# Performance work log

Measured on AMD Instinct MI355X. Metric: run time of the kernel, lower is better.

## Reference

```python
import jax, jax.numpy as jnp
import numpy as np

B, S, V, L, H, NH, NL = 4, 256, 64, 10, 128, 8, 3
DH = H // NH
LP1 = L + 1


def setup_inputs() -> dict:
    key = jax.random.key(0)
    ks = jax.random.split(key, 18)
    sc = 1.0 / np.sqrt(H)
    return {
        "x": jax.random.normal(ks[0], (B, S, V), jnp.float32),
        "adjacency_logits": jax.random.normal(ks[1], (V, V, LP1), jnp.float32) * 0.1,
        "var_emb": jax.random.normal(ks[2], (V, H), jnp.float32),
        "temp_emb": jax.random.normal(ks[3], (LP1, H), jnp.float32),
        "mech_W": jax.random.normal(ks[4], (V, NL, H, H), jnp.float32) * sc,
        "mech_b": jax.random.normal(ks[5], (V, NL, H), jnp.float32) * 0.01,
        "ln_g": jnp.ones((V, NL, H), jnp.float32),
        "ln_b": jnp.zeros((V, NL, H), jnp.float32),
        "Wq": jax.random.normal(ks[6], (V, H, H), jnp.float32) * sc,
        "Wk": jax.random.normal(ks[7], (V, H, H), jnp.float32) * sc,
        "Wv": jax.random.normal(ks[8], (V, H, H), jnp.float32) * sc,
        "Wo": jax.random.normal(ks[9], (V, H, H), jnp.float32) * sc,
        "bq": jnp.zeros((V, H), jnp.float32),
        "bk": jnp.zeros((V, H), jnp.float32),
        "bv": jnp.zeros((V, H), jnp.float32),
        "bo": jnp.zeros((V, H), jnp.float32),
        "out_W": jax.random.normal(ks[10], (V, H), jnp.float32) * sc,
        "out_b": jnp.zeros((V,), jnp.float32),
    }


def reference(x, adjacency_logits, var_emb, temp_emb, mech_W, mech_b, ln_g, ln_b,
              Wq, Wk, Wv, Wo, bq, bk, bv, bo, out_W, out_b):
    b, s, v = x.shape
    lp1 = adjacency_logits.shape[-1]
    adj = jax.nn.sigmoid(adjacency_logits)  # (V_src, V_tgt, L+1), soft adjacency

    # xlag[b,t,src,l] = x[b, t-l, src] with zero padding (the shift-pad loop, fused)
    xlag = jnp.stack([jnp.pad(x, ((0, 0), (l, 0), (0, 0)))[:, :s] for l in range(lp1)], axis=-1)

    # causal_input[b,t,tgt,h] = sum_{src,l} xlag * adj[src,tgt,l] * (var_emb[src,h] + temp_emb[l,h])
    A = jnp.einsum('btsl,sil->btis', xlag, adj)   # contracted over lag
    Bl = jnp.einsum('btsl,sil->btil', xlag, adj)  # contracted over source
    z = jnp.einsum('btis,sh->btih', A, var_emb) + jnp.einsum('btil,lh->btih', Bl, temp_emb)  # (B,S,V,H)

    # per-variable causal mechanism: Linear -> LayerNorm -> GELU (dropout = identity at eval)
    eps = 1e-5
    nl = mech_W.shape[1]
    for li in range(nl):
        z = jnp.einsum('btvh,vhk->btvk', z, mech_W[:, li]) + mech_b[:, li]
        mu = z.mean(axis=-1, keepdims=True)
        var = z.var(axis=-1, keepdims=True)
        z = (z - mu) / jnp.sqrt(var + eps) * ln_g[:, li] + ln_b[:, li]
        z = jax.nn.gelu(z, approximate=False)

    # per-variable multi-head self-attention over the sequence axis
    def heads(t):
        return t.reshape(b, s, v, NH, DH)
    q = heads(jnp.einsum('btvh,vhk->btvk', z, Wq) + bq)
    k = heads(jnp.einsum('btvh,vhk->btvk', z, Wk) + bk)
    vv = heads(jnp.einsum('btvh,vhk->btvk', z, Wv) + bv)
    scores = jnp.einsum('bqvnd,bkvnd->bvnqk', q, k) / np.sqrt(DH)  # (B,V,NH,S,S)
    attn = jax.nn.softmax(scores, axis=-1)
    o = jnp.einsum('bvnqk,bkvnd->bqvnd', attn, vv).reshape(b, s, v, NH * DH)
    o = jnp.einsum('btvh,vhk->btvk', o, Wo) + bo

    # per-variable output head Linear(H, 1), concatenated over variables
    predictions = jnp.einsum('btvh,vh->btv', o, out_W) + out_b  # (B,S,V)
    return predictions
```

## Files before the change

### kernel.cpp

```cpp
#include <hip/hip_runtime.h>
#include <math.h>

#define BB   4
#define SS   256
#define VV   64
#define LP1  11
#define HH   128
#define NHH  8
#define DHH  16
#define NLL  3
#define BSZ  1024

typedef unsigned short u16;
typedef unsigned int   u32;
typedef __attribute__((ext_vector_type(8))) short s16x8;
typedef __attribute__((ext_vector_type(4))) float f32x4;

__device__ __forceinline__ float bfbits2f(u32 hi16) {
    u32 i = hi16 << 16; float f; __builtin_memcpy(&f, &i, 4); return f;
}
__device__ __forceinline__ u16 f2bf(float f) {
    u32 i; __builtin_memcpy(&i, &f, 4);
    return (u16)((i + 0x7fffu + ((i >> 16) & 1u)) >> 16);
}
__device__ __forceinline__ u16 f2bf_trunc(float f) {
    u32 i; __builtin_memcpy(&i, &f, 4);
    return (u16)(i >> 16);
}
__device__ __forceinline__ u32 cvtpk(float lo, float hi) {
    u32 r;
    asm("v_cvt_pk_bf16_f32 %0, %1, %2" : "=v"(r) : "v"(lo), "v"(hi));
    return r;
}
__device__ __forceinline__ float ldf(const void* p, size_t i, int isbf) {
    if (isbf) return bfbits2f(((const u16*)p)[i]);
    return ((const float*)p)[i];
}
__device__ __forceinline__ float4 ld4(const void* p, size_t i, int isbf) {
    float4 v;
    if (isbf) {
        uint2 u = *(const uint2*)((const u16*)p + i);
        v.x = bfbits2f(u.x & 0xffffu); v.y = bfbits2f(u.x >> 16);
        v.z = bfbits2f(u.y & 0xffffu); v.w = bfbits2f(u.y >> 16);
    } else {
        v = *(const float4*)((const float*)p + i);
    }
    return v;
}
__device__ __forceinline__ void gll16(const u16* g, u16* l) {
    __builtin_amdgcn_global_load_lds(
        (const __attribute__((address_space(1))) void*)g,
        (__attribute__((address_space(3))) void*)l, 16, 0, 0);
}

__global__ __launch_bounds__(64) void k_sniff(const u16* __restrict__ probe,
                                              int* __restrict__ flags) {
    if (threadIdx.x == 0) {
        int wild = 0;
        for (int j = 0; j < 256; j++) {
            float v = bfbits2f(probe[j]);
            if (!(fabsf(v) < 1e8f)) wild = 1;
        }
        flags[0] = wild ? 0 : 1;
    }
}

__global__ __launch_bounds__(256) void k_adj(const void* __restrict__ logits,
                                             float* __restrict__ adj,
                                             const int* __restrict__ flags) {
    int isbf = flags[0];
    int i = blockIdx.x * 256 + threadIdx.x;
    if (i < VV * VV * LP1) {
        float v = ldf(logits, i, isbf);
        adj[i] = 1.f / (1.f + expf(-v));
    }
}

__global__ __launch_bounds__(128) void k_fuse(const void* __restrict__ Wo,
                                              const void* __restrict__ outW,
                                              const void* __restrict__ bo,
                                              const void* __restrict__ outb,
                                              float* __restrict__ wfused,
                                              float* __restrict__ bfused,
                                              const int* __restrict__ flags) {
    int isbf = flags[0];
    int v = blockIdx.x; int h = threadIdx.x;
    __shared__ float ow[HH];
    __shared__ float red[HH];
    ow[h] = ldf(outW, (size_t)v * HH + h, isbf);
    __syncthreads();
    size_t wb = ((size_t)v * HH + h) * HH;
    float acc = 0.f;
    #pragma unroll 8
    for (int k = 0; k < HH; k++) acc += ldf(Wo, wb + k, isbf) * ow[k];
    wfused[v * HH + h] = acc;
    red[h] = ldf(bo, (size_t)v * HH + h, isbf) * ow[h];
    __syncthreads();
    for (int s = 64; s > 0; s >>= 1) { if (h < s) red[h] += red[h + s]; __syncthreads(); }
    if (h == 0) bfused[v] = red[0] + ldf(outb, v, isbf);
}

struct WPack {
    const void* src[6];
    u16* dh[6];
    u16* dl[6];
};
#define TP 136
__global__ __launch_bounds__(256) void k_wprep(WPack wp,
                                               const int* __restrict__ flags) {
    int isbf = flags[0];
    int mat = blockIdx.x;
    int tid = threadIdx.x;
    if (mat >= 384) {
        if (mat == 384) {
            const void* raw = wp.src[4];
            u16* dh = wp.dh[4]; u16* dl = wp.dl[4];
            int n = tid >> 1, half = tid & 1;
            for (int i = 0; i < 32; i++) {
                int s = half * 32 + i;
                float val = ldf(raw, (size_t)s * HH + n, isbf);
                u16 hi = f2bf(val);
                int dst = n * 64 + (s ^ ((n & 7) * 8));
                dh[dst] = hi;
                dl[dst] = f2bf(val - bfbits2f(hi));
            }
        } else {
            const void* raw = wp.src[5];
            u16* dh = wp.dh[5]; u16* dl = wp.dl[5];
            for (int p = tid; p < 8192; p += 256) { dh[p] = 0; dl[p] = 0; }
            __syncthreads();
            if (tid < HH) {
                int n = tid;
                for (int l = 0; l < LP1; l++) {
                    float val = ldf(raw, (size_t)l * HH + n, isbf);
                    u16 hi = f2bf(val);
                    int dst = n * 64 + (l ^ ((n & 7) * 8));
                    dh[dst] = hi;
                    dl[dst] = f2bf(val - bfbits2f(hi));
                }
            }
        }
        return;
    }
    int seg = (mat < 192) ? 0 : 1 + ((mat - 192) >> 6);
    int rel = (mat < 192) ? mat : ((mat - 192) & 63);
    const void* raw = wp.src[seg];
    u16* Wh = wp.dh[seg];
    u16* Wl = wp.dl[seg];
    size_t src = (size_t)rel * (HH * HH);
    if (isbf) {
        __shared__ u16 tile[HH * TP];
        const uint4* sp = (const uint4*)((const u16*)raw + src);
        #pragma unroll
        for (int u = 0; u < 8; u++) {
            int p = u * 256 + tid;
            int h = p >> 4, k8 = (p & 15) * 8;
            int k8s = k8 ^ ((((u32)h >> 3) & 15) * 8);
            *(uint4*)&tile[h * TP + k8s] = sp[p];
        }
        __syncthreads();
        #pragma unroll
        for (int u = 0; u < 8; u++) {
            int p = u * 256 + tid;
            int kcol = p >> 4, h8 = (p & 15) * 8;
            u16 vals[8];
            #pragma unroll
            for (int j = 0; j < 8; j++) {
                int h = h8 + j;
                int ks = kcol ^ ((((u32)h >> 3) & 15) * 8);
                vals[j] = tile[h * TP + ks];
            }
            uint4 pk;
            pk.x = (u32)vals[0] | ((u32)vals[1] << 16);
            pk.y = (u32)vals[2] | ((u32)vals[3] << 16);
            pk.z = (u32)vals[4] | ((u32)vals[5] << 16);
            pk.w = (u32)vals[6] | ((u32)vals[7] << 16);
            int c = h8 >> 6;
            int kloc = (h8 & 63) ^ ((kcol & 7) * 8);
            *(uint4*)&Wh[src + c * 8192 + kcol * 64 + kloc] = pk;
        }
    } else {
        int kcol = tid >> 1, h0 = (tid & 1) * 64;
        for (int i = 0; i < 64; i++) {
            int h = h0 + i;
            float w = ldf(raw, src + (size_t)h * HH + kcol, 0);
            u16 hi = f2bf(w);
            int c = h >> 6;
            size_t dst = src + c * 8192 + (size_t)kcol * 64 + ((h & 63) ^ ((kcol & 7) * 8));
            Wh[dst] = hi;
            Wl[dst] = f2bf(w - bfbits2f(hi));
        }
    }
}

#define PB  72
__global__ __launch_bounds__(256) void k_mega(
    const void* __restrict__ x, const float* __restrict__ adjp,
    const u16* __restrict__ VeH, const u16* __restrict__ VeL,
    const u16* __restrict__ TeH, const u16* __restrict__ TeL,
    const u16* __restrict__ WmH, const u16* __restrict__ WmL,
    const u16* __restrict__ WqH, const u16* __restrict__ WqL,
    const u16* __restrict__ WkH, const u16* __restrict__ WkL,
    const u16* __restrict__ WvH, const u16* __restrict__ WvL,
    const void* __restrict__ mechb,
    const void* __restrict__ lng, const void* __restrict__ lnb,
    const void* __restrict__ bq, const void* __restrict__ bk,
    const void* __restrict__ bv,
    u16* __restrict__ Qh, u16* __restrict__ Ql,
    u16* __restrict__ Ko, u16* __restrict__ Vt,
    const int* __restrict__ flags)
{
    __shared__ __align__(16) u16 SMEM[32768];
    u16* Az_h = SMEM;
    u16* Az_l = SMEM + 8192;
    u16* Bd   = SMEM + 16384;
    u16* Vt_sh = Bd;

    int isbf = flags[0];
    int wexact = isbf;
    int tid = threadIdx.x;
    int bid = blockIdx.x;
    int xcd = bid & 7, idx = bid >> 3;
    int v = xcd * 8 + (idx >> 4);
    int tile = idx & 15;
    int b = tile >> 2, t0 = (tile & 3) * 64;
    int wave = tid >> 6, lane = tid & 63;
    int quad = lane >> 4, l15 = lane & 15;
    int m0 = wave * 16;
    int swzl = (l15 & 7) * 8;

    float* xt = (float*)SMEM;
    for (int p = tid; p < 74 * 64; p += 256) {
        int rr = p >> 6, s = p & 63;
        int trow = t0 - 10 + rr;
        float val = (trow >= 0) ? ldf(x, (size_t)(b * SS + trow) * VV + s, isbf) : 0.f;
        xt[s * 81 + rr] = val;
    }
    __syncthreads();

    float* A_f = (float*)Bd;
    float* Blp = A_f + 64 * 68;
    float* Blf = Blp + 64 * 44;
    {
        int t = lane;
        int sg = wave;
        float blp[LP1];
        #pragma unroll
        for (int l = 0; l < LP1; l++) blp[l] = 0.f;
        for (int k = 0; k < 16; k++) {
            int s = sg * 16 + k;
            const float* ap = adjp + (s * VV + v) * LP1;
            float xw[LP1];
            #pragma unroll
            for (int j = 0; j < LP1; j++) xw[j] = xt[s * 81 + t + j];
            float a = 0.f;
            #pragma unroll
            for (int l = 0; l < LP1; l++) {
                float pr = xw[10 - l] * ap[l];
                a += pr; blp[l] += pr;
            }
            A_f[t * 68 + s] = a;
        }
        #pragma unroll
        for (int l = 0; l < LP1; l++) Blp[t * 44 + sg * 11 + l] = blp[l];
    }
    __syncthreads();
    {
        int t = tid >> 2, c0 = (tid & 3) * 4;
        #pragma unroll
        for (int c = c0; c < c0 + 4; c++) {
            float s4 = 0.f;
            if (c < LP1)
                s4 = (Blp[t * 44 + c] + Blp[t * 44 + 11 + c]) +
                     (Blp[t * 44 + 22 + c] + Blp[t * 44 + 33 + c]);
            Blf[t * 16 + c] = s4;
        }
    }
    __syncthreads();

    s16x8 ahf[2], alf[2], blh, bll;
    #pragma unroll
    for (int kk = 0; kk < 2; kk++) {
        #pragma unroll
        for (int j = 0; j < 8; j++) {
            float a = A_f[(m0 + l15) * 68 + kk * 32 + quad * 8 + j];
            u32 w = cvtpk(a, a);
            u16 hi = (u16)(w & 0xffffu);
            ahf[kk][j] = (short)hi;
            float res = a - bfbits2f(hi);
            alf[kk][j] = (short)(cvtpk(res, res) & 0xffffu);
        }
    }
    #pragma unroll
    for (int j = 0; j < 8; j++) {
        float a = (quad < 2) ? Blf[(m0 + l15) * 16 + quad * 8 + j] : 0.f;
        u32 w = cvtpk(a, a);
        u16 hi = (u16)(w & 0xffffu);
        blh[j] = (short)hi;
        float res = a - bfbits2f(hi);
        bll[j] = (short)(cvtpk(res, res) & 0xffffu);
    }
    __syncthreads();

    auto stageB = [&](u16* dst, const u16* g) {
        const u16* gl = g + wave * 2048 + lane * 8;
        u16* lb = dst + wave * 2048;
        #pragma unroll
        for (int u = 0; u < 4; u++)
            gll16(gl + u * 512, lb + u * 512);
    };

    int shift = wexact ? 1 : 2;
    int PER = 1 << shift;
    int NCH = 6 << shift;

    auto wchunk = [&](int ch) -> const u16* {
        int li = ch >> shift;
        int sub = ch & (PER - 1);
        int cc = sub & 1, lo = sub >> 1;
        const u16* p; size_t wb;
        if (li < 3)       { p = lo ? WmL : WmH; wb = (size_t)(v * NLL + li) * 16384; }
        else if (li == 3) { p = lo ? WqL : WqH; wb = (size_t)v * 16384; }
        else if (li == 4) { p = lo ? WkL : WkH; wb = (size_t)v * 16384; }
        else              { p = lo ? WvL : WvH; wb = (size_t)v * 16384; }
        return p + wb + cc * 8192;
    };

    f32x4 acc[8];
    #pragma unroll
    for (int nt = 0; nt < 8; nt++) {
        f32x4 zz = {0.f, 0.f, 0.f, 0.f};
        acc[nt] = zz;
    }

    if (wexact) {
        stageB(Bd, VeH);
        stageB(Bd + 8192, TeH);
        asm volatile("s_waitcnt vmcnt(4) lgkmcnt(0)" ::: "memory");
        __builtin_amdgcn_s_barrier();
        __builtin_amdgcn_sched_barrier(0);
        __builtin_amdgcn_s_setprio(1);
        #pragma unroll
        for (int kk = 0; kk < 2; kk++) {
            int bcol = (kk * 32 + quad * 8) ^ swzl;
            #pragma unroll
            for (int nt = 0; nt < 8; nt++) {
                s16x8 bh = *(const s16x8*)&Bd[(nt * 16 + l15) * 64 + bcol];
                acc[nt] = __builtin_amdgcn_mfma_f32_16x16x32_bf16(ahf[kk], bh, acc[nt], 0, 0, 0);
                acc[nt] = __builtin_amdgcn_mfma_f32_16x16x32_bf16(alf[kk], bh, acc[nt], 0, 0, 0);
            }
        }
        __builtin_amdgcn_s_setprio(0);
        asm volatile("s_waitcnt vmcnt(0) lgkmcnt(0)" ::: "memory");
        __builtin_amdgcn_s_barrier();
        __builtin_amdgcn_sched_barrier(0);
        stageB(Bd, wchunk(0));
        __builtin_amdgcn_s_setprio(1);
        {
            int bcol = (quad * 8) ^ swzl;
            #pragma unroll
            for (int nt = 0; nt < 8; nt++) {
                s16x8 th = *(const s16x8*)&Bd[8192 + (nt * 16 + l15) * 64 + bcol];
                acc[nt] = __builtin_amdgcn_mfma_f32_16x16x32_bf16(blh, th, acc[nt], 0, 0, 0);
                acc[nt] = __builtin_amdgcn_mfma_f32_16x16x32_bf16(bll, th, acc[nt], 0, 0, 0);
            }
        }
        __builtin_amdgcn_s_setprio(0);
    } else {
        stageB(Bd, VeH);
        stageB(Bd + 8192, VeL);
        __syncthreads();
        #pragma unroll
        for (int kk = 0; kk < 2; kk++) {
            int bcol = (kk * 32 + quad * 8) ^ swzl;
            #pragma unroll
            for (int nt = 0; nt < 8; nt++) {
                s16x8 bh = *(const s16x8*)&Bd[(nt * 16 + l15) * 64 + bcol];
                s16x8 bl = *(const s16x8*)&Bd[8192 + (nt * 16 + l15) * 64 + bcol];
                acc[nt] = __builtin_amdgcn_mfma_f32_16x16x32_bf16(ahf[kk], bh, acc[nt], 0, 0, 0);
                acc[nt] = __builtin_amdgcn_mfma_f32_16x16x32_bf16(alf[kk], bh, acc[nt], 0, 0, 0);
                acc[nt] = __builtin_amdgcn_mfma_f32_16x16x32_bf16(ahf[kk], bl, acc[nt], 0, 0, 0);
            }
        }
        __syncthreads();
        stageB(Bd, TeH);
        stageB(Bd + 8192, TeL);
        __syncthreads();
        {
            int bcol = (quad * 8) ^ swzl;
            #pragma unroll
            for (int nt = 0; nt < 8; nt++) {
                s16x8 th = *(const s16x8*)&Bd[(nt * 16 + l15) * 64 + bcol];
                s16x8 tl = *(const s16x8*)&Bd[8192 + (nt * 16 + l15) * 64 + bcol];
                acc[nt] = __builtin_amdgcn_mfma_f32_16x16x32_bf16(blh, th, acc[nt], 0, 0, 0);
                acc[nt] = __builtin_amdgcn_mfma_f32_16x16x32_bf16(bll, th, acc[nt], 0, 0, 0);
                acc[nt] = __builtin_amdgcn_mfma_f32_16x16x32_bf16(blh, tl, acc[nt], 0, 0, 0);
            }
        }
        __syncthreads();
        stageB(Bd, wchunk(0));
    }

    #pragma unroll
    for (int r = 0; r < 4; r++) {
        int rloc = m0 + quad * 4 + r;
        int swr = (rloc & 7) * 8;
        #pragma unroll
        for (int nt = 0; nt < 8; nt++) {
            float val = acc[nt][r];
            float sx = __shfl_xor(val, 1);
            u32 w = cvtpk(val, sx);
            float res = val - bfbits2f(w & 0xffffu);
            float rx = __shfl_xor(res, 1);
            u32 wl = cvtpk(res, rx);
            if (!(l15 & 1)) {
                int colw = (nt * 16 + (l15 & ~1)) ^ swr;
                *(u32*)&Az_h[rloc * 128 + colw] = w;
                *(u32*)&Az_l[rloc * 128 + colw] = wl;
            }
        }
    }
    asm volatile("s_waitcnt lgkmcnt(0)" ::: "memory");
    __builtin_amdgcn_s_barrier();

    float bcol[8], gcol[8], b2col[8];

    auto epilogue = [&](int li) {
        if (li == 5) __syncthreads();
        #pragma unroll
        for (int r = 0; r < 4; r++) {
            float vals[8];
            float sum = 0.f, sq = 0.f;
            #pragma unroll
            for (int nt = 0; nt < 8; nt++) {
                float val = acc[nt][r] + bcol[nt];
                vals[nt] = val; sum += val; sq += val * val;
            }
            int rloc = m0 + quad * 4 + r;
            if (li < 3) {
                #pragma unroll
                for (int m = 1; m < 16; m <<= 1) {
                    sum += __shfl_xor(sum, m);
                    sq  += __shfl_xor(sq, m);
                }
                float mean = sum * (1.f / HH);
                float var  = sq * (1.f / HH) - mean * mean;
                float rstd = rsqrtf(var + 1e-5f);
                int swr = (rloc & 7) * 8;
                #pragma unroll
                for (int nt = 0; nt < 8; nt++) {
                    float y = (vals[nt] - mean) * rstd * gcol[nt] + b2col[nt];
                    y = 0.5f * y * (1.f + erff(y * 0.70710678118654752f));
                    float sx = __shfl_xor(y, 1);
                    u32 w = cvtpk(y, sx);
                    float res = y - bfbits2f(w & 0xffffu);
                    float rx = __shfl_xor(res, 1);
                    u32 wl = cvtpk(res, rx);
                    if (!(l15 & 1)) {
                        int colw = (nt * 16 + (l15 & ~1)) ^ swr;
                        *(u32*)&Az_h[rloc * 128 + colw] = w;
                        *(u32*)&Az_l[rloc * 128 + colw] = wl;
                    }
                }
            } else if (li == 3) {
                int row = tile * 64 + rloc;
                size_t ob = ((size_t)v * BSZ + row) * HH;
                #pragma unroll
                for (int nt = 0; nt < 8; nt++) {
                    float val = vals[nt];
                    float sx = __shfl_xor(val, 1);
                    u32 w = cvtpk(val, sx);
                    float res = val - bfbits2f(w & 0xffffu);
                    float rx = __shfl_xor(res, 1);
                    u32 wl = cvtpk(res, rx);
                    if (!(l15 & 1)) {
                        size_t oi = ob + nt * 16 + (l15 & ~1);
                        *(u32*)&Qh[oi] = w;
                        *(u32*)&Ql[oi] = wl;
                    }
                }
            } else if (li == 4) {
                int row = tile * 64 + rloc;
                size_t ob = ((size_t)v * BSZ + row) * HH;
                #pragma unroll
                for (int nt = 0; nt < 8; nt++) {
                    u32 h = f2bf(vals[nt]);
                    u32 hx = (u32)__shfl_xor((int)h, 1);
                    if (!(l15 & 1))
                        *(u32*)&Ko[ob + nt * 16 + (l15 & ~1)] = h | (hx << 16);
                }
            } else {
                #pragma unroll
                for (int nt = 0; nt < 8; nt++)
                    Vt_sh[(nt * 16 + l15) * PB + rloc] = f2bf(vals[nt]);
            }
        }
        if (li == 5) {
            __syncthreads();
            int col = tid >> 1, half = tid & 1;
            int n = col >> 4, d = col & 15;
            int bb = tile >> 2, tq = (tile & 3) * 64;
            size_t dst = (((size_t)(v * BB + bb) * NHH + n) * DHH + d) * SS + tq + half * 32;
            #pragma unroll
            for (int j = 0; j < 4; j++)
                *(uint4*)&Vt[dst + j * 8] = *(const uint4*)&Vt_sh[col * PB + half * 32 + j * 8];
        }
    };

    for (int ch = 0; ch < NCH; ch++) {
        int sub = ch & (PER - 1);
        int li = ch >> shift;
        int cc = sub & 1, lo = sub >> 1;

        if (ch + 1 < NCH) stageB(Bd + ((ch + 1) & 1) * 8192, wchunk(ch + 1));

        if (ch + 1 < NCH) asm volatile("s_waitcnt vmcnt(4) lgkmcnt(0)" ::: "memory");
        else              asm volatile("s_waitcnt vmcnt(0) lgkmcnt(0)" ::: "memory");
        __builtin_amdgcn_s_barrier();
        __builtin_amdgcn_sched_barrier(0);

        if (sub == 0) {
            #pragma unroll
            for (int nt = 0; nt < 8; nt++) {
                f32x4 zz = {0.f, 0.f, 0.f, 0.f};
                acc[nt] = zz;
            }
            #pragma unroll
            for (int nt = 0; nt < 8; nt++) {
                int col = nt * 16 + l15;
                if (li < 3) {
                    size_t pb = (size_t)v * (NLL * HH) + (size_t)li * HH + col;
                    bcol[nt]  = ldf(mechb, pb, isbf);
                    gcol[nt]  = ldf(lng, pb, isbf);
                    b2col[nt] = ldf(lnb, pb, isbf);
                } else {
                    const void* bp = (li == 3) ? bq : (li == 4) ? bk : bv;
                    bcol[nt] = ldf(bp, (size_t)v * HH + col, isbf);
                }
            }
        }

        const u16* Bp = Bd + (ch & 1) * 8192;
        __builtin_amdgcn_s_setprio(1);
        #pragma unroll
        for (int kk = 0; kk < 2; kk++) {
            int acol = (cc * 64 + kk * 32 + quad * 8) ^ swzl;
            int bcol2 = (kk * 32 + quad * 8) ^ swzl;
            s16x8 ah = *(const s16x8*)&Az_h[(m0 + l15) * 128 + acol];
            if (!lo) {
                s16x8 al = *(const s16x8*)&Az_l[(m0 + l15) * 128 + acol];
                #pragma unroll
                for (int nt = 0; nt < 8; nt++) {
                    s16x8 bh = *(const s16x8*)&Bp[(nt * 16 + l15) * 64 + bcol2];
                    acc[nt] = __builtin_amdgcn_mfma_f32_16x16x32_bf16(ah, bh, acc[nt], 0, 0, 0);
                    acc[nt] = __builtin_amdgcn_mfma_f32_16x16x32_bf16(al, bh, acc[nt], 0, 0, 0);
                }
            } else {
                #pragma unroll
                for (int nt = 0; nt < 8; nt++) {
                    s16x8 bl = *(const s16x8*)&Bp[(nt * 16 + l15) * 64 + bcol2];
                    acc[nt] = __builtin_amdgcn_mfma_f32_16x16x32_bf16(ah, bl, acc[nt], 0, 0, 0);
                }
            }
        }
        __builtin_amdgcn_s_setprio(0);

        if (sub == PER - 1) epilogue(li);

        asm volatile("s_waitcnt lgkmcnt(0)" ::: "memory");
        __builtin_amdgcn_s_barrier();
    }
}

#define LDW 40
__global__ __launch_bounds__(256) void k_attn2(const u16* __restrict__ Qh,
                                               const u16* __restrict__ Ql,
                                               const u16* __restrict__ K16,
                                               const u16* __restrict__ Vt,
                                               float* __restrict__ O) {
    __shared__ u16 Kp_sh[SS * LDW];
    __shared__ u16 Vt_sh[DHH * 264];
    __shared__ u16 P_sh[4][16 * LDW];
    int tid = threadIdx.x;
    int wave = tid >> 6, lane = tid & 63;
    int quad = lane >> 4, l15 = lane & 15;
    int bn = blockIdx.x, v = blockIdx.y;
    int b = bn >> 3, n = bn & 7;
    size_t qkbase = ((size_t)v * BSZ + b * SS) * HH + n * DHH;
    size_t vtbase = ((size_t)(v * BB + b) * NHH + n) * DHH * SS;

    {
        int row = tid;
        uint4 k0 = *(const uint4*)&K16[qkbase + (size_t)row * HH];
        uint4 k1 = *(const uint4*)&K16[qkbase + (size_t)row * HH + 8];
        *(uint4*)&Kp_sh[row * LDW + 0]  = k0;
        *(uint4*)&Kp_sh[row * LDW + 8]  = k1;
        *(uint4*)&Kp_sh[row * LDW + 16] = k0;
        *(uint4*)&Kp_sh[row * LDW + 24] = k1;
    }
    #pragma unroll
    for (int u = 0; u < 2; u++) {
        int p = u * 256 + tid;
        int d = p >> 5, su = (p & 31) * 8;
        *(uint4*)&Vt_sh[d * 264 + su] = *(const uint4*)&Vt[vtbase + (size_t)d * SS + su];
    }
    __syncthreads();

    s16x8 ones;
    #pragma unroll
    for (int i = 0; i < 8; i++) ones[i] = (short)0x3F80;

    for (int mt = wave * 4; mt < wave * 4 + 4; mt++) {
        const u16* Qsrc = (quad < 2) ? Qh : Ql;
        s16x8 aq = *(const s16x8*)&Qsrc[qkbase + (size_t)(mt * 16 + l15) * HH + (quad & 1) * 8];
        f32x4 oacc = {0.f, 0.f, 0.f, 0.f};
        f32x4 lacc = {0.f, 0.f, 0.f, 0.f};
        for (int jt2 = 0; jt2 < 8; jt2++) {
            #pragma unroll
            for (int sub = 0; sub < 2; sub++) {
                int jt = jt2 * 2 + sub;
                s16x8 bk = *(const s16x8*)&Kp_sh[(jt * 16 + l15) * LDW + quad * 8];
                f32x4 s = {0.f, 0.f, 0.f, 0.f};
                s = __builtin_amdgcn_mfma_f32_16x16x32_bf16(aq, bk, s, 0, 0, 0);
                #pragma unroll
                for (int r = 0; r < 4; r++) {
                    float p = __expf(s[r] * 0.25f);
                    P_sh[wave][(quad * 4 + r) * LDW + sub * 16 + l15] = f2bf_trunc(p);
                }
            }
            s16x8 ap = *(const s16x8*)&P_sh[wave][l15 * LDW + quad * 8];
            s16x8 bv = *(const s16x8*)&Vt_sh[l15 * 264 + jt2 * 32 + quad * 8];
            oacc = __builtin_amdgcn_mfma_f32_16x16x32_bf16(ap, bv, oacc, 0, 0, 0);
            lacc = __builtin_amdgcn_mfma_f32_16x16x32_bf16(ap, ones, lacc, 0, 0, 0);
        }
        #pragma unroll
        for (int r = 0; r < 4; r++) {
            float val = oacc[r] / lacc[r];
            O[((size_t)v * BSZ + b * SS + mt * 16 + quad * 4 + r) * HH + n * DHH + l15] = val;
        }
    }
}

__global__ __launch_bounds__(256) void k_final(const float* __restrict__ o,
                                               const float* __restrict__ wfused,
                                               const float* __restrict__ bfused,
                                               void* __restrict__ out,
                                               const int* __restrict__ flags) {
    __shared__ float wf[HH];
    int isbf = flags[0];
    int tid = threadIdx.x; int b = blockIdx.x; int v = blockIdx.y;
    if (tid < HH) wf[tid] = wfused[v * HH + tid];
    __syncthreads();
    int rg = tid >> 3;
    int l8 = tid & 7;
    float4 w0 = *(const float4*)&wf[l8 * 16];
    float4 w1 = *(const float4*)&wf[l8 * 16 + 4];
    float4 w2 = *(const float4*)&wf[l8 * 16 + 8];
    float4 w3 = *(const float4*)&wf[l8 * 16 + 12];
    float bv = bfused[v];
    #pragma unroll
    for (int pass = 0; pass < 8; pass++) {
        int bt = b * SS + pass * 32 + rg;
        const float4* orow = (const float4*)(o + ((size_t)v * BSZ + bt) * HH + l8 * 16);
        float4 a0 = orow[0], a1 = orow[1], a2 = orow[2], a3 = orow[3];
        float acc = a0.x * w0.x + a0.y * w0.y + a0.z * w0.z + a0.w * w0.w
                  + a1.x * w1.x + a1.y * w1.y + a1.z * w1.z + a1.w * w1.w
                  + a2.x * w2.x + a2.y * w2.y + a2.z * w2.z + a2.w * w2.w
                  + a3.x * w3.x + a3.y * w3.y + a3.z * w3.z + a3.w * w3.w;
        acc += __shfl_xor(acc, 1);
        acc += __shfl_xor(acc, 2);
        acc += __shfl_xor(acc, 4);
        if (l8 == 0) {
            float pred = acc + bv;
            size_t oi = (size_t)bt * VV + v;
            if (isbf) ((u16*)out)[oi] = f2bf(pred);
            else      ((float*)out)[oi] = pred;
        }
    }
}

extern "C" void kernel_launch(void* const* d_in, const int* in_sizes, int n_in,
                              void* d_out, int out_size, void* d_ws, size_t ws_size,
                              hipStream_t stream) {
    (void)out_size; (void)ws_size;

    static const int dict_sizes[18]  = {65536,45056,8192,1408,3145728,24576,24576,24576,
                                        1048576,1048576,1048576,1048576,8192,8192,8192,8192,8192,64};
    static const int alpha_sizes[18] = {1048576,1048576,1048576,1048576,45056,8192,8192,8192,
                                        8192,24576,24576,3145728,24576,8192,64,1408,8192,65536};
    static const int alpha_pos[18]   = {17,4,16,15,11,12,10,9,2,0,3,1,7,5,8,6,13,14};
    static const int alpha_logical[18] = {9,11,8,10,1,13,15,12,14,7,6,4,5,16,17,3,2,0};

    const void* in[18];
    bool is_dict = (n_in == 18), is_alpha = (n_in == 18);
    for (int i = 0; i < 18 && i < n_in; i++) {
        if (in_sizes[i] != dict_sizes[i])  is_dict = false;
        if (in_sizes[i] != alpha_sizes[i]) is_alpha = false;
    }
    if (is_dict) {
        for (int i = 0; i < 18; i++) in[i] = d_in[i];
    } else if (is_alpha) {
        for (int i = 0; i < 18; i++) in[i] = d_in[alpha_pos[i]];
    } else {
        bool used[18] = {false};
        for (int a = 0; a < 18; a++) {
            int lg = alpha_logical[a];
            for (int i = 0; i < n_in && i < 18; i++) {
                if (!used[i] && in_sizes[i] == dict_sizes[lg]) {
                    in[lg] = d_in[i]; used[i] = true; break;
                }
            }
        }
    }

    const void* x        = in[0];
    const void* adjl     = in[1];
    const void* var_emb  = in[2];
    const void* temp_emb = in[3];
    const void* mechW    = in[4];
    const void* mechb    = in[5];
    const void* lng      = in[6];
    const void* lnb      = in[7];
    const void* Wq       = in[8];
    const void* Wk       = in[9];
    const void* Wv       = in[10];
    const void* Wo       = in[11];
    const void* bq       = in[12];
    const void* bk       = in[13];
    const void* bv       = in[14];
    const void* bo       = in[15];
    const void* outW     = in[16];
    const void* outb     = in[17];

    float* ws     = (float*)d_ws;
    int*   flags  = (int*)ws;
    float* adj    = ws + 32;
    float* wfused = ws + 45088;
    float* bfused = ws + 53280;
    float* Obuf   = ws + 53376;
    u16*   zhB    = (u16*)(ws + 8441984);
    u16*   zlB    = (u16*)(ws + 12636288);
    u16*   K16    = (u16*)(ws + 16830592);
    u16*   Vt16   = (u16*)(ws + 21024896);
    u16*   WtmH   = (u16*)(ws + 25219200);
    u16*   WtmL   = (u16*)(ws + 26792064);
    u16*   WtqH   = (u16*)(ws + 28364928);
    u16*   WtqL   = (u16*)(ws + 28889216);
    u16*   WtkH   = (u16*)(ws + 29413504);
    u16*   WtkL   = (u16*)(ws + 29937792);
    u16*   WtvH   = (u16*)(ws + 30462080);
    u16*   WtvL   = (u16*)(ws + 30986368);
    u16*   WveH   = (u16*)(ws + 31510656);
    u16*   WveL   = (u16*)(ws + 31514752);
    u16*   WteH   = (u16*)(ws + 31518848);
    u16*   WteL   = (u16*)(ws + 31522944);

    k_sniff <<<dim3(1),    dim3(64),  0, stream>>>((const u16*)mechW, flags);
    k_adj   <<<dim3(176),  dim3(256), 0, stream>>>(adjl, adj, flags);
    k_fuse  <<<dim3(64),   dim3(128), 0, stream>>>(Wo, outW, bo, outb, wfused, bfused, flags);

    WPack wp;
    wp.src[0] = mechW;    wp.dh[0] = WtmH; wp.dl[0] = WtmL;
    wp.src[1] = Wq;       wp.dh[1] = WtqH; wp.dl[1] = WtqL;
    wp.src[2] = Wk;       wp.dh[2] = WtkH; wp.dl[2] = WtkL;
    wp.src[3] = Wv;       wp.dh[3] = WtvH; wp.dl[3] = WtvL;
    wp.src[4] = var_emb;  wp.dh[4] = WveH; wp.dl[4] = WveL;
    wp.src[5] = temp_emb; wp.dh[5] = WteH; wp.dl[5] = WteL;
    k_wprep <<<dim3(386),  dim3(256), 0, stream>>>(wp, flags);

    k_mega<<<dim3(1024), dim3(256), 0, stream>>>(
            x, adj,
            WveH, WveL, WteH, WteL,
            WtmH, WtmL, WtqH, WtqL, WtkH, WtkL, WtvH, WtvL,
            mechb, lng, lnb, bq, bk, bv,
            zhB, zlB, K16, Vt16, flags);

    k_attn2 <<<dim3(BB * NHH, VV), dim3(256), 0, stream>>>(zhB, zlB, K16, Vt16, Obuf);
    k_final <<<dim3(BB, VV), dim3(256), 0, stream>>>(Obuf, wfused, bfused, d_out, flags);
}
```

Baseline: 418.4 us.

## Split k_mega N dimension across 8 waves with cross-wave LayerNorm reduction

Doubles k_mega's block to 512 threads. Each of the 8 waves now computes a 16-row by 64-column output slice, splitting the 128 output columns between two wave groups, so each wave holds half the accumulators and issues half the MFMAs. LayerNorm statistics are now combined across the two column halves through a small shared-memory reduction buffer plus an extra barrier. The front-end lag contraction is also restructured: adjacency is staged into LDS and the source-contracted term is computed directly instead of via per-wave partials. The aim is more latency hiding and lower register pressure per wave, at the cost of extra barriers and slightly more LDS.

```diff
diff --git a/kernel.cpp b/kernel.cpp
--- a/kernel.cpp
+++ b/kernel.cpp
@@ -35,17 +35,6 @@
 __device__ __forceinline__ float ldf(const void* p, size_t i, int isbf) {
     if (isbf) return bfbits2f(((const u16*)p)[i]);
     return ((const float*)p)[i];
-}
-__device__ __forceinline__ float4 ld4(const void* p, size_t i, int isbf) {
-    float4 v;
-    if (isbf) {
-        uint2 u = *(const uint2*)((const u16*)p + i);
-        v.x = bfbits2f(u.x & 0xffffu); v.y = bfbits2f(u.x >> 16);
-        v.z = bfbits2f(u.y & 0xffffu); v.w = bfbits2f(u.y >> 16);
-    } else {
-        v = *(const float4*)((const float*)p + i);
-    }
-    return v;
 }
 __device__ __forceinline__ void gll16(const u16* g, u16* l) {
     __builtin_amdgcn_global_load_lds(
@@ -194,7 +183,7 @@
 }
 
 #define PB  72
-__global__ __launch_bounds__(256) void k_mega(
+__global__ __launch_bounds__(512) void k_mega(
     const void* __restrict__ x, const float* __restrict__ adjp,
     const u16* __restrict__ VeH, const u16* __restrict__ VeL,
     const u16* __restrict__ TeH, const u16* __restrict__ TeL,
@@ -210,10 +199,11 @@
     u16* __restrict__ Ko, u16* __restrict__ Vt,
     const int* __restrict__ flags)
 {
-    __shared__ __align__(16) u16 SMEM[32768];
+    __shared__ __align__(16) u16 SMEM[33280];
     u16* Az_h = SMEM;
     u16* Az_l = SMEM + 8192;
     u16* Bd   = SMEM + 16384;
+    float* red = (float*)(SMEM + 32768);
     u16* Vt_sh = Bd;
 
     int isbf = flags[0];
@@ -226,55 +216,46 @@
     int b = tile >> 2, t0 = (tile & 3) * 64;
     int wave = tid >> 6, lane = tid & 63;
     int quad = lane >> 4, l15 = lane & 15;
-    int m0 = wave * 16;
+    int m0 = (wave & 3) * 16;
+    int ch2 = wave >> 2;
+    int chb = ch2 * 64;
     int swzl = (l15 & 7) * 8;
 
     float* xt = (float*)SMEM;
-    for (int p = tid; p < 74 * 64; p += 256) {
+    float* adjL = xt + 64 * 81;
+    for (int p = tid; p < 74 * 64; p += 512) {
         int rr = p >> 6, s = p & 63;
         int trow = t0 - 10 + rr;
-        float val = (trow >= 0) ? ldf(x, (size_t)(b * SS + trow) * VV + s, isbf) : 0.f;
-        xt[s * 81 + rr] = val;
+        xt[s * 81 + rr] = (trow >= 0) ? ldf(x, (size_t)(b * SS + trow) * VV + s, isbf) : 0.f;
+    }
+    for (int p = tid; p < 64 * LP1; p += 512) {
+        int s = p / LP1, l = p - s * LP1;
+        adjL[s * 12 + l] = adjp[(s * VV + v) * LP1 + l];
     }
     __syncthreads();
 
     float* A_f = (float*)Bd;
-    float* Blp = A_f + 64 * 68;
-    float* Blf = Blp + 64 * 44;
+    float* Blf = A_f + 64 * 68;
     {
         int t = lane;
-        int sg = wave;
-        float blp[LP1];
-        #pragma unroll
-        for (int l = 0; l < LP1; l++) blp[l] = 0.f;
-        for (int k = 0; k < 16; k++) {
-            int s = sg * 16 + k;
-            const float* ap = adjp + (s * VV + v) * LP1;
-            float xw[LP1];
-            #pragma unroll
-            for (int j = 0; j < LP1; j++) xw[j] = xt[s * 81 + t + j];
+        #pragma unroll
+        for (int i = 0; i < 8; i++) {
+            int s = wave * 8 + i;
             float a = 0.f;
             #pragma unroll
-            for (int l = 0; l < LP1; l++) {
-                float pr = xw[10 - l] * ap[l];
-                a += pr; blp[l] += pr;
-            }
+            for (int l = 0; l < LP1; l++)
+                a += xt[s * 81 + t + 10 - l] * adjL[s * 12 + l];
             A_f[t * 68 + s] = a;
         }
-        #pragma unroll
-        for (int l = 0; l < LP1; l++) Blp[t * 44 + sg * 11 + l] = blp[l];
-    }
-    __syncthreads();
-    {
-        int t = tid >> 2, c0 = (tid & 3) * 4;
-        #pragma unroll
-        for (int c = c0; c < c0 + 4; c++) {
-            float s4 = 0.f;
-            if (c < LP1)
-                s4 = (Blp[t * 44 + c] + Blp[t * 44 + 11 + c]) +
-                     (Blp[t * 44 + 22 + c] + Blp[t * 44 + 33 + c]);
-            Blf[t * 16 + c] = s4;
-        }
+    }
+    for (int pp = tid; pp < 64 * 16; pp += 512) {
+        int t = pp >> 4, l = pp & 15;
+        float a = 0.f;
+        if (l < LP1) {
+            for (int s = 0; s < 64; s++)
+                a += xt[s * 81 + t + 10 - l] * adjL[s * 12 + l];
+        }
+        Blf[t * 16 + l] = a;
     }
     __syncthreads();
 
@@ -303,11 +284,10 @@
     __syncthreads();
 
     auto stageB = [&](u16* dst, const u16* g) {
-        const u16* gl = g + wave * 2048 + lane * 8;
-        u16* lb = dst + wave * 2048;
-        #pragma unroll
-        for (int u = 0; u < 4; u++)
-            gll16(gl + u * 512, lb + u * 512);
+        const u16* gl = g + wave * 1024 + lane * 8;
+        u16* lb = dst + wave * 1024;
+        gll16(gl, lb);
+        gll16(gl + 512, lb + 512);
     };
 
     int shift = wexact ? 1 : 2;
@@ -326,9 +306,9 @@
         return p + wb + cc * 8192;
     };
 
-    f32x4 acc[8];
+    f32x4 acc[4];
     #pragma unroll
-    for (int nt = 0; nt < 8; nt++) {
+    for (int nt = 0; nt < 4; nt++) {
         f32x4 zz = {0.f, 0.f, 0.f, 0.f};
         acc[nt] = zz;
     }
@@ -336,16 +316,16 @@
     if (wexact) {
         stageB(Bd, VeH);
         stageB(Bd + 8192, TeH);
-        asm volatile("s_waitcnt vmcnt(4) lgkmcnt(0)" ::: "memory");
+        asm volatile("s_waitcnt vmcnt(2) lgkmcnt(0)" ::: "memory");
         __builtin_amdgcn_s_barrier();
         __builtin_amdgcn_sched_barrier(0);
         __builtin_amdgcn_s_setprio(1);
         #pragma unroll
         for (int kk = 0; kk < 2; kk++) {
-            int bcol = (kk * 32 + quad * 8) ^ swzl;
-            #pragma unroll
-            for (int nt = 0; nt < 8; nt++) {
-                s16x8 bh = *(const s16x8*)&Bd[(nt * 16 + l15) * 64 + bcol];
+            int bcolv = (kk * 32 + quad * 8) ^ swzl;
+            #pragma unroll
+            for (int nt = 0; nt < 4; nt++) {
+                s16x8 bh = *(const s16x8*)&Bd[(chb + nt * 16 + l15) * 64 + bcolv];
                 acc[nt] = __builtin_amdgcn_mfma_f32_16x16x32_bf16(ahf[kk], bh, acc[nt], 0, 0, 0);
                 acc[nt] = __builtin_amdgcn_mfma_f32_16x16x32_bf16(alf[kk], bh, acc[nt], 0, 0, 0);
             }
@@ -357,10 +337,10 @@
         stageB(Bd, wchunk(0));
         __builtin_amdgcn_s_setprio(1);
         {
-            int bcol = (quad * 8) ^ swzl;
-            #pragma unroll
-            for (int nt = 0; nt < 8; nt++) {
-                s16x8 th = *(const s16x8*)&Bd[8192 + (nt * 16 + l15) * 64 + bcol];
+            int bcolv = (quad * 8) ^ swzl;
+            #pragma unroll
+            for (int nt = 0; nt < 4; nt++) {
+                s16x8 th = *(const s16x8*)&Bd[8192 + (chb + nt * 16 + l15) * 64 + bcolv];
                 acc[nt] = __builtin_amdgcn_mfma_f32_16x16x32_bf16(blh, th, acc[nt], 0, 0, 0);
                 acc[nt] = __builtin_amdgcn_mfma_f32_16x16x32_bf16(bll, th, acc[nt], 0, 0, 0);
             }
@@ -372,11 +352,11 @@
         __syncthreads();
         #pragma unroll
         for (int kk = 0; kk < 2; kk++) {
-            int bcol = (kk * 32 + quad * 8) ^ swzl;
-            #pragma unroll
-            for (int nt = 0; nt < 8; nt++) {
-                s16x8 bh = *(const s16x8*)&Bd[(nt * 16 + l15) * 64 + bcol];
-                s16x8 bl = *(const s16x8*)&Bd[8192 + (nt * 16 + l15) * 64 + bcol];
+            int bcolv = (kk * 32 + quad * 8) ^ swzl;
+            #pragma unroll
+            for (int nt = 0; nt < 4; nt++) {
+                s16x8 bh = *(const s16x8*)&Bd[(chb + nt * 16 + l15) * 64 + bcolv];
+                s16x8 bl = *(const s16x8*)&Bd[8192 + (chb + nt * 16 + l15) * 64 + bcolv];
                 acc[nt] = __builtin_amdgcn_mfma_f32_16x16x32_bf16(ahf[kk], bh, acc[nt], 0, 0, 0);
                 acc[nt] = __builtin_amdgcn_mfma_f32_16x16x32_bf16(alf[kk], bh, acc[nt], 0, 0, 0);
                 acc[nt] = __builtin_amdgcn_mfma_f32_16x16x32_bf16(ahf[kk], bl, acc[nt], 0, 0, 0);
@@ -387,11 +367,11 @@
         stageB(Bd + 8192, TeL);
         __syncthreads();
         {
-            int bcol = (quad * 8) ^ swzl;
-            #pragma unroll
-            for (int nt = 0; nt < 8; nt++) {
-                s16x8 th = *(const s16x8*)&Bd[(nt * 16 + l15) * 64 + bcol];
-                s16x8 tl = *(const s16x8*)&Bd[8192 + (nt * 16 + l15) * 64 + bcol];
+            int bcolv = (quad * 8) ^ swzl;
+            #pragma unroll
+            for (int nt = 0; nt < 4; nt++) {
+                s16x8 th = *(const s16x8*)&Bd[(chb + nt * 16 + l15) * 64 + bcolv];
+                s16x8 tl = *(const s16x8*)&Bd[8192 + (chb + nt * 16 + l15) * 64 + bcolv];
                 acc[nt] = __builtin_amdgcn_mfma_f32_16x16x32_bf16(blh, th, acc[nt], 0, 0, 0);
                 acc[nt] = __builtin_amdgcn_mfma_f32_16x16x32_bf16(bll, th, acc[nt], 0, 0, 0);
                 acc[nt] = __builtin_amdgcn_mfma_f32_16x16x32_bf16(blh, tl, acc[nt], 0, 0, 0);
@@ -406,7 +386,7 @@
         int rloc = m0 + quad * 4 + r;
         int swr = (rloc & 7) * 8;
         #pragma unroll
-        for (int nt = 0; nt < 8; nt++) {
+        for (int nt = 0; nt < 4; nt++) {
             float val = acc[nt][r];
             float sx = __shfl_xor(val, 1);
             u32 w = cvtpk(val, sx);
@@ -414,7 +394,7 @@
             float rx = __shfl_xor(res, 1);
             u32 wl = cvtpk(res, rx);
             if (!(l15 & 1)) {
-                int colw = (nt * 16 + (l15 & ~1)) ^ swr;
+                int colw = (chb + nt * 16 + (l15 & ~1)) ^ swr;
                 *(u32*)&Az_h[rloc * 128 + colw] = w;
                 *(u32*)&Az_l[rloc * 128 + colw] = wl;
             }
@@ -423,33 +403,49 @@
     asm volatile("s_waitcnt lgkmcnt(0)" ::: "memory");
     __builtin_amdgcn_s_barrier();
 
-    float bcol[8], gcol[8], b2col[8];
+    float bcol[4], gcol[4], b2col[4];
 
     auto epilogue = [&](int li) {
         if (li == 5) __syncthreads();
-        #pragma unroll
-        for (int r = 0; r < 4; r++) {
-            float vals[8];
-            float sum = 0.f, sq = 0.f;
-            #pragma unroll
-            for (int nt = 0; nt < 8; nt++) {
-                float val = acc[nt][r] + bcol[nt];
-                vals[nt] = val; sum += val; sq += val * val;
-            }
-            int rloc = m0 + quad * 4 + r;
-            if (li < 3) {
+        if (li < 3) {
+            float vals[4][4], psum[4], psq[4];
+            #pragma unroll
+            for (int r = 0; r < 4; r++) {
+                float sum = 0.f, sq = 0.f;
+                #pragma unroll
+                for (int nt = 0; nt < 4; nt++) {
+                    float val = acc[nt][r] + bcol[nt];
+                    vals[r][nt] = val; sum += val; sq += val * val;
+                }
                 #pragma unroll
                 for (int m = 1; m < 16; m <<= 1) {
                     sum += __shfl_xor(sum, m);
                     sq  += __shfl_xor(sq, m);
                 }
-                float mean = sum * (1.f / HH);
-                float var  = sq * (1.f / HH) - mean * mean;
+                psum[r] = sum; psq[r] = sq;
+            }
+            if (l15 == 0) {
+                #pragma unroll
+                for (int r = 0; r < 4; r++) {
+                    int row = m0 + quad * 4 + r;
+                    red[row * 4 + ch2 * 2]     = psum[r];
+                    red[row * 4 + ch2 * 2 + 1] = psq[r];
+                }
+            }
+            asm volatile("s_waitcnt lgkmcnt(0)" ::: "memory");
+            __builtin_amdgcn_s_barrier();
+            #pragma unroll
+            for (int r = 0; r < 4; r++) {
+                int rloc = m0 + quad * 4 + r;
+                float st = psum[r] + red[rloc * 4 + (ch2 ^ 1) * 2];
+                float qt = psq[r]  + red[rloc * 4 + (ch2 ^ 1) * 2 + 1];
+                float mean = st * (1.f / HH);
+                float var  = qt * (1.f / HH) - mean * mean;
                 float rstd = rsqrtf(var + 1e-5f);
                 int swr = (rloc & 7) * 8;
                 #pragma unroll
-                for (int nt = 0; nt < 8; nt++) {
-                    float y = (vals[nt] - mean) * rstd * gcol[nt] + b2col[nt];
+                for (int nt = 0; nt < 4; nt++) {
+                    float y = (vals[r][nt] - mean) * rstd * gcol[nt] + b2col[nt];
                     y = 0.5f * y * (1.f + erff(y * 0.70710678118654752f));
                     float sx = __shfl_xor(y, 1);
                     u32 w = cvtpk(y, sx);
@@ -457,53 +453,61 @@
                     float rx = __shfl_xor(res, 1);
                     u32 wl = cvtpk(res, rx);
                     if (!(l15 & 1)) {
-                        int colw = (nt * 16 + (l15 & ~1)) ^ swr;
+                        int colw = (chb + nt * 16 + (l15 & ~1)) ^ swr;
                         *(u32*)&Az_h[rloc * 128 + colw] = w;
                         *(u32*)&Az_l[rloc * 128 + colw] = wl;
                     }
                 }
-            } else if (li == 3) {
-                int row = tile * 64 + rloc;
-                size_t ob = ((size_t)v * BSZ + row) * HH;
+            }
+        } else {
+            #pragma unroll
+            for (int r = 0; r < 4; r++) {
+                int rloc = m0 + quad * 4 + r;
+                float vals4[4];
                 #pragma unroll
-                for (int nt = 0; nt < 8; nt++) {
-                    float val = vals[nt];
-                    float sx = __shfl_xor(val, 1);
-                    u32 w = cvtpk(val, sx);
-                    float res = val - bfbits2f(w & 0xffffu);
-                    float rx = __shfl_xor(res, 1);
-                    u32 wl = cvtpk(res, rx);
-                    if (!(l15 & 1)) {
-                        size_t oi = ob + nt * 16 + (l15 & ~1);
-                        *(u32*)&Qh[oi] = w;
-                        *(u32*)&Ql[oi] = wl;
+                for (int nt = 0; nt < 4; nt++) vals4[nt] = acc[nt][r] + bcol[nt];
+                if (li == 3) {
+                    int row = tile * 64 + rloc;
+                    size_t ob = ((size_t)v * BSZ + row) * HH;
+                    #pragma unroll
+                    for (int nt = 0; nt < 4; nt++) {
+                        float val = vals4[nt];
+                        float sx = __shfl_xor(val, 1);
+                        u32 w = cvtpk(val, sx);
+                        float res = val - bfbits2f(w & 0xffffu);
+                        float rx = __shfl_xor(res, 1);
+                        u32 wl = cvtpk(res, rx);
+                        if (!(l15 & 1)) {
+                            size_t oi = ob + chb + nt * 16 + (l15 & ~1);
+                            *(u32*)&Qh[oi] = w;
+                            *(u32*)&Ql[oi] = wl;
+                        }
                     }
-                }
-            } else if (li == 4) {
-                int row = tile * 64 + rloc;
-                size_t ob = ((size_t)v * BSZ + row) * HH;
-                #pragma unroll
-                for (int nt = 0; nt < 8; nt++) {
-                    u32 h = f2bf(vals[nt]);
-                    u32 hx = (u32)__shfl_xor((int)h, 1);
-                    if (!(l15 & 1))
-                        *(u32*)&Ko[ob + nt * 16 + (l15 & ~1)] = h | (hx << 16);
-                }
-            } else {
-                #pragma unroll
-                for (int nt = 0; nt < 8; nt++)
-                    Vt_sh[(nt * 16 + l15) * PB + rloc] = f2bf(vals[nt]);
+                } else if (li == 4) {
+                    int row = tile * 64 + rloc;
+                    size_t ob = ((size_t)v * BSZ + row) * HH;
+                    #pragma unroll
+                    for (int nt = 0; nt < 4; nt++) {
+                        u32 h = f2bf(vals4[nt]);
+                        u32 hx = (u32)__shfl_xor((int)h, 1);
+                        if (!(l15 & 1))
+                            *(u32*)&Ko[ob + chb + nt * 16 + (l15 & ~1)] = h | (hx << 16);
+                    }
+                } else {
+                    #pragma unroll
+                    for (int nt = 0; nt < 4; nt++)
+                        Vt_sh[(chb + nt * 16 + l15) * PB + rloc] = f2bf(vals4[nt]);
+                }
             }
         }
         if (li == 5) {
             __syncthreads();
-            int col = tid >> 1, half = tid & 1;
+            int col = tid >> 2, q4 = tid & 3;
             int n = col >> 4, d = col & 15;
             int bb = tile >> 2, tq = (tile & 3) * 64;
-            size_t dst = (((size_t)(v * BB + bb) * NHH + n) * DHH + d) * SS + tq + half * 32;
-            #pragma unroll
-            for (int j = 0; j < 4; j++)
-                *(uint4*)&Vt[dst + j * 8] = *(const uint4*)&Vt_sh[col * PB + half * 32 + j * 8];
+            size_t dst = (((size_t)(v * BB + bb) * NHH + n) * DHH + d) * SS + tq + q4 * 16;
+            *(uint4*)&Vt[dst]     = *(const uint4*)&Vt_sh[col * PB + q4 * 16];
+            *(uint4*)&Vt[dst + 8] = *(const uint4*)&Vt_sh[col * PB + q4 * 16 + 8];
         }
     };
 
@@ -514,20 +518,20 @@
 
         if (ch + 1 < NCH) stageB(Bd + ((ch + 1) & 1) * 8192, wchunk(ch + 1));
 
-        if (ch + 1 < NCH) asm volatile("s_waitcnt vmcnt(4) lgkmcnt(0)" ::: "memory");
+        if (ch + 1 < NCH) asm volatile("s_waitcnt vmcnt(2) lgkmcnt(0)" ::: "memory");
         else              asm volatile("s_waitcnt vmcnt(0) lgkmcnt(0)" ::: "memory");
         __builtin_amdgcn_s_barrier();
         __builtin_amdgcn_sched_barrier(0);
 
         if (sub == 0) {
             #pragma unroll
-            for (int nt = 0; nt < 8; nt++) {
+            for (int nt = 0; nt < 4; nt++) {
                 f32x4 zz = {0.f, 0.f, 0.f, 0.f};
                 acc[nt] = zz;
             }
             #pragma unroll
-            for (int nt = 0; nt < 8; nt++) {
-                int col = nt * 16 + l15;
+            for (int nt = 0; nt < 4; nt++) {
+                int col = chb + nt * 16 + l15;
                 if (li < 3) {
                     size_t pb = (size_t)v * (NLL * HH) + (size_t)li * HH + col;
                     bcol[nt]  = ldf(mechb, pb, isbf);
@@ -550,15 +554,15 @@
             if (!lo) {
                 s16x8 al = *(const s16x8*)&Az_l[(m0 + l15) * 128 + acol];
                 #pragma unroll
-                for (int nt = 0; nt < 8; nt++) {
-                    s16x8 bh = *(const s16x8*)&Bp[(nt * 16 + l15) * 64 + bcol2];
+                for (int nt = 0; nt < 4; nt++) {
+                    s16x8 bh = *(const s16x8*)&Bp[(chb + nt * 16 + l15) * 64 + bcol2];
                     acc[nt] = __builtin_amdgcn_mfma_f32_16x16x32_bf16(ah, bh, acc[nt], 0, 0, 0);
                     acc[nt] = __builtin_amdgcn_mfma_f32_16x16x32_bf16(al, bh, acc[nt], 0, 0, 0);
                 }
             } else {
                 #pragma unroll
-                for (int nt = 0; nt < 8; nt++) {
-                    s16x8 bl = *(const s16x8*)&Bp[(nt * 16 + l15) * 64 + bcol2];
+                for (int nt = 0; nt < 4; nt++) {
+                    s16x8 bl = *(const s16x8*)&Bp[(chb + nt * 16 + l15) * 64 + bcol2];
                     acc[nt] = __builtin_amdgcn_mfma_f32_16x16x32_bf16(ah, bl, acc[nt], 0, 0, 0);
                 }
             }
@@ -768,7 +772,7 @@
     wp.src[5] = temp_emb; wp.dh[5] = WteH; wp.dl[5] = WteL;
     k_wprep <<<dim3(386),  dim3(256), 0, stream>>>(wp, flags);
 
-    k_mega<<<dim3(1024), dim3(256), 0, stream>>>(
+    k_mega<<<dim3(1024), dim3(512), 0, stream>>>(
             x, adj,
             WveH, WveL, WteH, WteL,
             WtmH, WtmL, WtqH, WtqL, WtkH, WtkL, WtvH, WtvL,
```

Result: slower. 481.9 us (+15.2%).
